# Optimization experiments

Hardware: AMD Instinct MI355X
Metric: run time of the kernel (lower is better)

## Reference

```python
import jax, jax.numpy as jnp
import numpy as np

N_NODES = 50000
N_EDGES = 800000
IN_FEATS = 64
K = 4
OUT_FEATS = 256


def setup_inputs() -> dict:
    key = jax.random.key(0)
    k1, k2, k3, k4, k5 = jax.random.split(key, 5)
    signal = jax.random.normal(k1, (N_NODES, IN_FEATS), dtype=jnp.float32)
    src = jax.random.randint(k2, (N_EDGES,), 0, N_NODES, dtype=jnp.int32)
    dst = jax.random.randint(k3, (N_EDGES,), 0, N_NODES, dtype=jnp.int32)
    lambda_max = jnp.array([2.0], dtype=jnp.float32)  # normalized Laplacian bound
    W = jax.random.normal(k4, (IN_FEATS * K, OUT_FEATS), dtype=jnp.float32) * (1.0 / np.sqrt(IN_FEATS * K))
    b = jax.random.normal(k5, (OUT_FEATS,), dtype=jnp.float32) * 0.01
    return {"signal": signal, "src": src, "dst": dst, "lambda_max": lambda_max, "W": W, "b": b}


def reference(signal, src, dst, lambda_max, W, b):
    n = signal.shape[0]
    # in-degrees, clamped to >= 1, then D^{-1/2}
    deg = jax.ops.segment_sum(jnp.ones_like(dst, dtype=signal.dtype), dst, num_segments=n)
    d_sqrt = jnp.power(jnp.clip(deg, 1.0), -0.5)[:, None]  # [N,1]

    def unn_laplacian(x):
        # D^{-1/2} A D^{-1/2} x via gather-from-src, scatter-sum-to-dst
        h = (x * d_sqrt)[src]                                   # [E,f]
        agg = jax.ops.segment_sum(h, dst, num_segments=n)       # [N,f]
        return agg * d_sqrt

    X0 = signal
    Xs = [X0]
    if K > 1:
        re_norm = 2.0 / lambda_max  # broadcasts over nodes ([1] -> [N,f])
        X1 = -re_norm * unn_laplacian(X0) + X0 * (re_norm - 1.0)
        Xs.append(X1)
        for _ in range(2, K):
            Xi = -2.0 * re_norm * unn_laplacian(X1) + X1 * 2.0 * (re_norm - 1.0) - X0
            Xs.append(Xi)
            X1, X0 = Xi, X1
    Xt = jnp.concatenate(Xs, axis=1)  # [N, f*K]
    return jax.nn.relu(Xt @ W + b)
```

## Files before the change

kernel.cpp:

```cpp
#include <hip/hip_runtime.h>

#define NN 50000
#define NE 800000
#define F  64
#define FK 256
#define OUTF 256
#define CAP 48
#define NT 3128

#define NPART 8
#define PART_NODES 6250
#define FILL_CHUNKS 256
#define CHUNK_E 3125

typedef __attribute__((ext_vector_type(8))) short s16x8;
typedef __attribute__((ext_vector_type(4))) float f32x4;

static __device__ __forceinline__ unsigned short f2bf(float f) {
    unsigned u = __float_as_uint(f);
    u += 0x7fffu + ((u >> 16) & 1u);
    return (unsigned short)(u >> 16);
}
static __device__ __forceinline__ float bf2f(int h) {
    return __uint_as_float(((unsigned)(h & 0xffff)) << 16);
}

__global__ __launch_bounds__(256) void fill_kernel(const int* __restrict__ src,
                                                   const int* __restrict__ dst,
                                                   int* __restrict__ cnt,
                                                   int* __restrict__ csr) {
    int part  = blockIdx.x & (NPART - 1);
    int chunk = blockIdx.x >> 3;
    int lo = part * PART_NODES;
    int e0 = chunk * CHUNK_E;
    int e1 = e0 + CHUNK_E;
    for (int e = e0 + threadIdx.x; e < e1; e += 256) {
        int d = dst[e];
        if ((unsigned)(d - lo) < (unsigned)PART_NODES) {
            int s = src[e];
            int k = atomicAdd(&cnt[d], 1);
            if (k < CAP) csr[d * CAP + k] = s;
        }
    }
}

__global__ void dsqrt_kernel(const int* __restrict__ cnt, float* __restrict__ dsq) {
    int n = blockIdx.x * blockDim.x + threadIdx.x;
    if (n < NN) dsq[n] = rsqrtf(fmaxf((float)cnt[n], 1.0f));
}


__global__ void copy0_kernel(const float* __restrict__ sig,
                             const float* __restrict__ dsq,
                             unsigned short* __restrict__ XrowH,
                             unsigned short* __restrict__ XrowL,
                             unsigned short* __restrict__ XfH) {
    int i = blockIdx.x * blockDim.x + threadIdx.x;
    if (i >= NN * 16) return;
    int n = i >> 4, fq = i & 15;
    float d = dsq[n];
    float4 v = *(const float4*)&sig[n * F + fq * 4];
    float yx = v.x * d, yy = v.y * d, yz = v.z * d, yw = v.w * d;
    unsigned short h0 = f2bf(yx), h1 = f2bf(yy), h2 = f2bf(yz), h3 = f2bf(yw);
    unsigned short l0 = f2bf(yx - bf2f(h0)), l1 = f2bf(yy - bf2f(h1));
    unsigned short l2 = f2bf(yz - bf2f(h2)), l3 = f2bf(yw - bf2f(h3));
    *(ushort4*)&XrowH[(size_t)n * 192 + fq * 4] = make_ushort4(h0, h1, h2, h3);
    *(ushort4*)&XrowL[(size_t)n * 192 + fq * 4] = make_ushort4(l0, l1, l2, l3);
    unsigned short u0 = f2bf(v.x), u1 = f2bf(v.y), u2 = f2bf(v.z), u3 = f2bf(v.w);
    int t = n >> 4, m = n & 15;
    int k0 = fq >> 3, qq = (fq >> 1) & 3, half = fq & 1;
    size_t base = ((size_t)((t * 8 + k0) * 64 + qq * 16 + m)) * 8 + half * 4;
    *(ushort4*)&XfH[base] = make_ushort4(u0, u1, u2, u3);
}

__global__ void convw_kernel(const float* __restrict__ W,
                             unsigned short* __restrict__ WfH,
                             unsigned short* __restrict__ WfL) {
    int id = blockIdx.x * blockDim.x + threadIdx.x;
    if (id >= 8192) return;
    int lane = id & 63, k0 = (id >> 6) & 7, ct = id >> 9;
    int n = lane & 15, q = lane >> 4;
    s16x8 h, l;
    #pragma unroll
    for (int j = 0; j < 8; ++j) {
        float x = W[(k0 * 32 + q * 8 + j) * OUTF + ct * 16 + n];
        unsigned short hh = f2bf(x);
        h[j] = (short)hh;
        l[j] = (short)f2bf(x - bf2f(hh));
    }
    ((s16x8*)WfH)[id] = h;
    ((s16x8*)WfL)[id] = l;
}

__global__ __launch_bounds__(256) void lap_kernel(const int* __restrict__ cnt,
                                                  const int* __restrict__ csr,
                                                  const float* __restrict__ dsq,
                                                  const float* __restrict__ lm,
                                                  unsigned short* __restrict__ XrowH,
                                                  unsigned short* __restrict__ XrowL,
                                                  unsigned short* __restrict__ XfH, int p) {
    int lane = threadIdx.x & 63;
    int half = lane >> 5;
    int sub  = lane & 31;
    int q2   = sub >> 4;
    int fq   = sub & 15;
    int wid  = (blockIdx.x * blockDim.x + threadIdx.x) >> 6;
    int n    = wid * 2 + half;
    if (n >= NN) return;
    int dgf = cnt[n];
    int dg  = min(dgf, CAP);
    int cin = p - 1;
    int foff = fq << 2;

    float ax = 0.f, ay = 0.f, az = 0.f, aw = 0.f;
    for (int k = 0; k < dg; k += 16) {
        int   s[8];
        float w[8];
        ushort4 h[8];
        #pragma unroll
        for (int j = 0; j < 8; ++j) {
            int slot = k + q2 + 2 * j;
            int ok   = slot < dg;
            int si   = csr[n * CAP + slot];
            s[j] = ok ? si : 0;
            w[j] = ok ? 1.0f : 0.0f;
        }
        #pragma unroll
        for (int j = 0; j < 8; ++j)
            h[j] = *(const ushort4*)&XrowH[((size_t)s[j] * 3 + cin) * 64 + foff];
        #pragma unroll
        for (int j = 0; j < 8; ++j) {
            ax += bf2f(h[j].x) * w[j];
            ay += bf2f(h[j].y) * w[j];
            az += bf2f(h[j].z) * w[j];
            aw += bf2f(h[j].w) * w[j];
        }
    }
    ax += __shfl_xor(ax, 16);
    ay += __shfl_xor(ay, 16);
    az += __shfl_xor(az, 16);
    aw += __shfl_xor(aw, 16);

    float rn = 2.0f / lm[0];
    float dn = dsq[n];
    float sq = sqrtf(fmaxf((float)dgf, 1.0f));
    ushort4 xh = *(const ushort4*)&XrowH[((size_t)n * 3 + cin) * 64 + foff];
    ushort4 xl = *(const ushort4*)&XrowL[((size_t)n * 3 + cin) * 64 + foff];
    float x1x = (bf2f(xh.x) + bf2f(xl.x)) * sq;
    float x1y = (bf2f(xh.y) + bf2f(xl.y)) * sq;
    float x1z = (bf2f(xh.z) + bf2f(xl.z)) * sq;
    float x1w = (bf2f(xh.w) + bf2f(xl.w)) * sq;
    float rx, ry, rz, rw;
    if (p == 1) {
        float c1 = rn - 1.0f;
        rx = -rn * dn * ax + x1x * c1;
        ry = -rn * dn * ay + x1y * c1;
        rz = -rn * dn * az + x1z * c1;
        rw = -rn * dn * aw + x1w * c1;
    } else {
        ushort4 zh = *(const ushort4*)&XrowH[((size_t)n * 3 + (p - 2)) * 64 + foff];
        ushort4 zl = *(const ushort4*)&XrowL[((size_t)n * 3 + (p - 2)) * 64 + foff];
        float c1 = 2.0f * (rn - 1.0f);
        rx = -2.0f * rn * dn * ax + x1x * c1 - (bf2f(zh.x) + bf2f(zl.x)) * sq;
        ry = -2.0f * rn * dn * ay + x1y * c1 - (bf2f(zh.y) + bf2f(zl.y)) * sq;
        rz = -2.0f * rn * dn * az + x1z * c1 - (bf2f(zh.z) + bf2f(zl.z)) * sq;
        rw = -2.0f * rn * dn * aw + x1w * c1 - (bf2f(zh.w) + bf2f(zl.w)) * sq;
    }

    float yx = rx * dn, yy = ry * dn, yz = rz * dn, yw = rw * dn;
    unsigned short yh0 = f2bf(yx), yh1 = f2bf(yy), yh2 = f2bf(yz), yh3 = f2bf(yw);
    if (q2 == 0) {
        if (p < 3)
            *(ushort4*)&XrowH[((size_t)n * 3 + p) * 64 + foff] = make_ushort4(yh0, yh1, yh2, yh3);
        unsigned short u0 = f2bf(rx), u1 = f2bf(ry), u2 = f2bf(rz), u3 = f2bf(rw);
        int t = n >> 4, m = n & 15;
        int k0 = p * 2 + (fq >> 3), qq = (fq >> 1) & 3, hf = fq & 1;
        size_t fbase = ((size_t)((t * 8 + k0) * 64 + qq * 16 + m)) * 8 + hf * 4;
        *(ushort4*)&XfH[fbase] = make_ushort4(u0, u1, u2, u3);
    } else if (p < 3) {
        unsigned short l0 = f2bf(yx - bf2f(yh0)), l1 = f2bf(yy - bf2f(yh1));
        unsigned short l2 = f2bf(yz - bf2f(yh2)), l3 = f2bf(yw - bf2f(yh3));
        *(ushort4*)&XrowL[((size_t)n * 3 + p) * 64 + foff] = make_ushort4(l0, l1, l2, l3);
    }
}

__global__ __launch_bounds__(512, 2) void gemm_kernel(const unsigned short* __restrict__ XfH,
                                                      const unsigned short* __restrict__ WfH,
                                                      const unsigned short* __restrict__ WfL,
                                                      const float* __restrict__ b,
                                                      float* __restrict__ out) {
    int lane = threadIdx.x & 63;
    int w    = threadIdx.x >> 6;
    int rh = w & 1, cg = w >> 1;
    int m = lane & 15, q = lane >> 4;
    int bt0 = blockIdx.x * 4;
    const s16x8* AH = (const s16x8*)XfH;
    const s16x8* BH = (const s16x8*)WfH;
    const s16x8* BL = (const s16x8*)WfL;

    f32x4 acc[2][4];
    #pragma unroll
    for (int rt = 0; rt < 2; ++rt)
        #pragma unroll
        for (int c = 0; c < 4; ++c) acc[rt][c] = (f32x4){0.f, 0.f, 0.f, 0.f};

    #pragma unroll
    for (int k0 = 0; k0 < 8; ++k0) {
        s16x8 a[2];
        #pragma unroll
        for (int rt = 0; rt < 2; ++rt)
            a[rt] = AH[((bt0 + rh * 2 + rt) * 8 + k0) * 64 + lane];
        #pragma unroll
        for (int c = 0; c < 4; ++c) {
            int ct = cg * 4 + c;
            s16x8 bh = BH[(ct * 8 + k0) * 64 + lane];
            s16x8 bl = BL[(ct * 8 + k0) * 64 + lane];
            #pragma unroll
            for (int rt = 0; rt < 2; ++rt) {
                acc[rt][c] = __builtin_amdgcn_mfma_f32_16x16x32_bf16(a[rt], bh, acc[rt][c], 0, 0, 0);
                acc[rt][c] = __builtin_amdgcn_mfma_f32_16x16x32_bf16(a[rt], bl, acc[rt][c], 0, 0, 0);
            }
        }
    }

    #pragma unroll
    for (int rt = 0; rt < 2; ++rt) {
        int rbase = (bt0 + rh * 2 + rt) * 16 + q * 4;
        #pragma unroll
        for (int c = 0; c < 4; ++c) {
            int col = (cg * 4 + c) * 16 + m;
            float bv = b[col];
            #pragma unroll
            for (int i = 0; i < 4; ++i) {
                int r = rbase + i;
                if (r < NN) out[r * OUTF + col] = fmaxf(acc[rt][c][i] + bv, 0.0f);
            }
        }
    }
}

extern "C" void kernel_launch(void* const* d_in, const int* in_sizes, int n_in,
                              void* d_out, int out_size, void* d_ws, size_t ws_size,
                              hipStream_t stream) {
    const float* signal     = (const float*)d_in[0];
    const int*   src        = (const int*)  d_in[1];
    const int*   dst        = (const int*)  d_in[2];
    const float* lambda_max = (const float*)d_in[3];
    const float* W          = (const float*)d_in[4];
    const float* b          = (const float*)d_in[5];
    float* out = (float*)d_out;

    int*   cnt = (int*)d_ws;
    int*   csr = cnt + NN;
    float* dsq = (float*)(csr + NN * CAP);
    unsigned short* XrowH = (unsigned short*)(dsq + NN);
    unsigned short* XrowL = XrowH + (size_t)NN * 192;
    unsigned short* XfH   = XrowL + (size_t)NN * 192;
    unsigned short* WfH   = XfH + (size_t)NT * 4096;
    unsigned short* WfL   = WfH + 65536;

    hipMemsetAsync(cnt, 0, NN * sizeof(int), stream);
    fill_kernel<<<NPART * FILL_CHUNKS, 256, 0, stream>>>(src, dst, cnt, csr);
    dsqrt_kernel<<<(NN + 255) / 256, 256, 0, stream>>>(cnt, dsq);
    copy0_kernel<<<(NN * 16 + 255) / 256, 256, 0, stream>>>(signal, dsq, XrowH, XrowL, XfH);
    convw_kernel<<<32, 256, 0, stream>>>(W, WfH, WfL);

    for (int p = 1; p <= 3; ++p)
        lap_kernel<<<NN / 8, 256, 0, stream>>>(cnt, csr, dsq, lambda_max, XrowH, XrowL, XfH, p);

    gemm_kernel<<<782, 512, 0, stream>>>(XfH, WfH, WfL, b, out);
}
```

Baseline: 232.7 us.

## Switch GEMM to single fp16 MFMA, fuse prep kernels, enlarge GEMM tile

The GEMM operands move from bf16 to fp16. W is no longer split into high and low bf16 halves, so the GEMM issues one MFMA per tile instead of two. The dsqrt, copy0 and convw kernels are merged into one prep kernel, and both prep and lap now recompute D^{-1/2} from the counts instead of reading a separate array. Each GEMM block now covers 8 row tiles instead of 4, so half as many blocks are launched. The fp16 path gives a narrower exponent range than bf16 and the larger tile increases register pressure and lowers the block count.

```diff
diff --git a/kernel.cpp b/kernel.cpp
--- a/kernel.cpp
+++ b/kernel.cpp
@@ -3,7 +3,6 @@
 #define NN 50000
 #define NE 800000
 #define F  64
-#define FK 256
 #define OUTF 256
 #define CAP 48
 #define NT 3128
@@ -13,8 +12,9 @@
 #define FILL_CHUNKS 256
 #define CHUNK_E 3125
 
-typedef __attribute__((ext_vector_type(8))) short s16x8;
-typedef __attribute__((ext_vector_type(4))) float f32x4;
+typedef __attribute__((ext_vector_type(8))) short    s16x8;
+typedef __attribute__((ext_vector_type(8))) _Float16 f16x8;
+typedef __attribute__((ext_vector_type(4))) float    f32x4;
 
 static __device__ __forceinline__ unsigned short f2bf(float f) {
     unsigned u = __float_as_uint(f);
@@ -23,6 +23,10 @@
 }
 static __device__ __forceinline__ float bf2f(int h) {
     return __uint_as_float(((unsigned)(h & 0xffff)) << 16);
+}
+static __device__ __forceinline__ unsigned short f2h(float f) {
+    _Float16 h = (_Float16)f;
+    return __builtin_bit_cast(unsigned short, h);
 }
 
 __global__ __launch_bounds__(256) void fill_kernel(const int* __restrict__ src,
@@ -44,61 +48,53 @@
     }
 }
 
-__global__ void dsqrt_kernel(const int* __restrict__ cnt, float* __restrict__ dsq) {
-    int n = blockIdx.x * blockDim.x + threadIdx.x;
-    if (n < NN) dsq[n] = rsqrtf(fmaxf((float)cnt[n], 1.0f));
-}
-
-
-__global__ void copy0_kernel(const float* __restrict__ sig,
-                             const float* __restrict__ dsq,
-                             unsigned short* __restrict__ XrowH,
-                             unsigned short* __restrict__ XrowL,
-                             unsigned short* __restrict__ XfH) {
-    int i = blockIdx.x * blockDim.x + threadIdx.x;
-    if (i >= NN * 16) return;
-    int n = i >> 4, fq = i & 15;
-    float d = dsq[n];
-    float4 v = *(const float4*)&sig[n * F + fq * 4];
-    float yx = v.x * d, yy = v.y * d, yz = v.z * d, yw = v.w * d;
-    unsigned short h0 = f2bf(yx), h1 = f2bf(yy), h2 = f2bf(yz), h3 = f2bf(yw);
-    unsigned short l0 = f2bf(yx - bf2f(h0)), l1 = f2bf(yy - bf2f(h1));
-    unsigned short l2 = f2bf(yz - bf2f(h2)), l3 = f2bf(yw - bf2f(h3));
-    *(ushort4*)&XrowH[(size_t)n * 192 + fq * 4] = make_ushort4(h0, h1, h2, h3);
-    *(ushort4*)&XrowL[(size_t)n * 192 + fq * 4] = make_ushort4(l0, l1, l2, l3);
-    unsigned short u0 = f2bf(v.x), u1 = f2bf(v.y), u2 = f2bf(v.z), u3 = f2bf(v.w);
-    int t = n >> 4, m = n & 15;
-    int k0 = fq >> 3, qq = (fq >> 1) & 3, half = fq & 1;
-    size_t base = ((size_t)((t * 8 + k0) * 64 + qq * 16 + m)) * 8 + half * 4;
-    *(ushort4*)&XfH[base] = make_ushort4(u0, u1, u2, u3);
-}
-
-__global__ void convw_kernel(const float* __restrict__ W,
-                             unsigned short* __restrict__ WfH,
-                             unsigned short* __restrict__ WfL) {
-    int id = blockIdx.x * blockDim.x + threadIdx.x;
-    if (id >= 8192) return;
-    int lane = id & 63, k0 = (id >> 6) & 7, ct = id >> 9;
-    int n = lane & 15, q = lane >> 4;
-    s16x8 h, l;
-    #pragma unroll
-    for (int j = 0; j < 8; ++j) {
-        float x = W[(k0 * 32 + q * 8 + j) * OUTF + ct * 16 + n];
-        unsigned short hh = f2bf(x);
-        h[j] = (short)hh;
-        l[j] = (short)f2bf(x - bf2f(hh));
-    }
-    ((s16x8*)WfH)[id] = h;
-    ((s16x8*)WfL)[id] = l;
+
+__global__ __launch_bounds__(256) void prep_kernel(const float* __restrict__ sig,
+                                                   const int* __restrict__ cnt,
+                                                   const float* __restrict__ W,
+                                                   unsigned short* __restrict__ XrowH,
+                                                   unsigned short* __restrict__ XrowL,
+                                                   unsigned short* __restrict__ XfF,
+                                                   unsigned short* __restrict__ WfF) {
+    int bid = blockIdx.x;
+    if (bid < 3125) {
+        int i = bid * 256 + threadIdx.x;
+        int n = i >> 4, fq = i & 15;
+        float d = rsqrtf(fmaxf((float)cnt[n], 1.0f));
+        float4 v = *(const float4*)&sig[n * F + fq * 4];
+        float yx = v.x * d, yy = v.y * d, yz = v.z * d, yw = v.w * d;
+        unsigned short h0 = f2bf(yx), h1 = f2bf(yy), h2 = f2bf(yz), h3 = f2bf(yw);
+        unsigned short l0 = f2bf(yx - bf2f(h0)), l1 = f2bf(yy - bf2f(h1));
+        unsigned short l2 = f2bf(yz - bf2f(h2)), l3 = f2bf(yw - bf2f(h3));
+        *(ushort4*)&XrowH[(size_t)n * 192 + fq * 4] = make_ushort4(h0, h1, h2, h3);
+        *(ushort4*)&XrowL[(size_t)n * 192 + fq * 4] = make_ushort4(l0, l1, l2, l3);
+        unsigned short u0 = f2h(v.x), u1 = f2h(v.y), u2 = f2h(v.z), u3 = f2h(v.w);
+        int t = n >> 4, m = n & 15;
+        int k0 = fq >> 3, qq = (fq >> 1) & 3, half = fq & 1;
+        size_t base = ((size_t)((t * 8 + k0) * 64 + qq * 16 + m)) * 8 + half * 4;
+        *(ushort4*)&XfF[base] = make_ushort4(u0, u1, u2, u3);
+    } else {
+        int id = (bid - 3125) * 256 + threadIdx.x;
+        if (id < 8192) {
+            int lane = id & 63, k0 = (id >> 6) & 7, ct = id >> 9;
+            int n = lane & 15, q = lane >> 4;
+            s16x8 h;
+            #pragma unroll
+            for (int j = 0; j < 8; ++j) {
+                float x = W[(k0 * 32 + q * 8 + j) * OUTF + ct * 16 + n];
+                h[j] = (short)f2h(x);
+            }
+            ((s16x8*)WfF)[id] = h;
+        }
+    }
 }
 
 __global__ __launch_bounds__(256) void lap_kernel(const int* __restrict__ cnt,
                                                   const int* __restrict__ csr,
-                                                  const float* __restrict__ dsq,
                                                   const float* __restrict__ lm,
                                                   unsigned short* __restrict__ XrowH,
                                                   unsigned short* __restrict__ XrowL,
-                                                  unsigned short* __restrict__ XfH, int p) {
+                                                  unsigned short* __restrict__ XfF, int p) {
     int lane = threadIdx.x & 63;
     int half = lane >> 5;
     int sub  = lane & 31;
@@ -142,7 +138,7 @@
     aw += __shfl_xor(aw, 16);
 
     float rn = 2.0f / lm[0];
-    float dn = dsq[n];
+    float dn = rsqrtf(fmaxf((float)dgf, 1.0f));
     float sq = sqrtf(fmaxf((float)dgf, 1.0f));
     ushort4 xh = *(const ushort4*)&XrowH[((size_t)n * 3 + cin) * 64 + foff];
     ushort4 xl = *(const ushort4*)&XrowL[((size_t)n * 3 + cin) * 64 + foff];
@@ -172,11 +168,11 @@
     if (q2 == 0) {
         if (p < 3)
             *(ushort4*)&XrowH[((size_t)n * 3 + p) * 64 + foff] = make_ushort4(yh0, yh1, yh2, yh3);
-        unsigned short u0 = f2bf(rx), u1 = f2bf(ry), u2 = f2bf(rz), u3 = f2bf(rw);
+        unsigned short u0 = f2h(rx), u1 = f2h(ry), u2 = f2h(rz), u3 = f2h(rw);
         int t = n >> 4, m = n & 15;
         int k0 = p * 2 + (fq >> 3), qq = (fq >> 1) & 3, hf = fq & 1;
         size_t fbase = ((size_t)((t * 8 + k0) * 64 + qq * 16 + m)) * 8 + hf * 4;
-        *(ushort4*)&XfH[fbase] = make_ushort4(u0, u1, u2, u3);
+        *(ushort4*)&XfF[fbase] = make_ushort4(u0, u1, u2, u3);
     } else if (p < 3) {
         unsigned short l0 = f2bf(yx - bf2f(yh0)), l1 = f2bf(yy - bf2f(yh1));
         unsigned short l2 = f2bf(yz - bf2f(yh2)), l3 = f2bf(yw - bf2f(yh3));
@@ -184,48 +180,43 @@
     }
 }
 
-__global__ __launch_bounds__(512, 2) void gemm_kernel(const unsigned short* __restrict__ XfH,
-                                                      const unsigned short* __restrict__ WfH,
-                                                      const unsigned short* __restrict__ WfL,
+__global__ __launch_bounds__(512, 2) void gemm_kernel(const unsigned short* __restrict__ XfF,
+                                                      const unsigned short* __restrict__ WfF,
                                                       const float* __restrict__ b,
                                                       float* __restrict__ out) {
     int lane = threadIdx.x & 63;
     int w    = threadIdx.x >> 6;
     int rh = w & 1, cg = w >> 1;
     int m = lane & 15, q = lane >> 4;
-    int bt0 = blockIdx.x * 4;
-    const s16x8* AH = (const s16x8*)XfH;
-    const s16x8* BH = (const s16x8*)WfH;
-    const s16x8* BL = (const s16x8*)WfL;
-
-    f32x4 acc[2][4];
+    int bt0 = blockIdx.x * 8;
+    const f16x8* A = (const f16x8*)XfF;
+    const f16x8* B = (const f16x8*)WfF;
+
+    f32x4 acc[4][4];
     #pragma unroll
-    for (int rt = 0; rt < 2; ++rt)
+    for (int rt = 0; rt < 4; ++rt)
         #pragma unroll
         for (int c = 0; c < 4; ++c) acc[rt][c] = (f32x4){0.f, 0.f, 0.f, 0.f};
 
     #pragma unroll
     for (int k0 = 0; k0 < 8; ++k0) {
-        s16x8 a[2];
-        #pragma unroll
-        for (int rt = 0; rt < 2; ++rt)
-            a[rt] = AH[((bt0 + rh * 2 + rt) * 8 + k0) * 64 + lane];
+        f16x8 a[4];
+        #pragma unroll
+        for (int rt = 0; rt < 4; ++rt)
+            a[rt] = A[((bt0 + rh * 4 + rt) * 8 + k0) * 64 + lane];
         #pragma unroll
         for (int c = 0; c < 4; ++c) {
             int ct = cg * 4 + c;
-            s16x8 bh = BH[(ct * 8 + k0) * 64 + lane];
-            s16x8 bl = BL[(ct * 8 + k0) * 64 + lane];
+            f16x8 bh = B[(ct * 8 + k0) * 64 + lane];
             #pragma unroll
-            for (int rt = 0; rt < 2; ++rt) {
-                acc[rt][c] = __builtin_amdgcn_mfma_f32_16x16x32_bf16(a[rt], bh, acc[rt][c], 0, 0, 0);
-                acc[rt][c] = __builtin_amdgcn_mfma_f32_16x16x32_bf16(a[rt], bl, acc[rt][c], 0, 0, 0);
-            }
+            for (int rt = 0; rt < 4; ++rt)
+                acc[rt][c] = __builtin_amdgcn_mfma_f32_16x16x32_f16(a[rt], bh, acc[rt][c], 0, 0, 0);
         }
     }
 
     #pragma unroll
-    for (int rt = 0; rt < 2; ++rt) {
-        int rbase = (bt0 + rh * 2 + rt) * 16 + q * 4;
+    for (int rt = 0; rt < 4; ++rt) {
+        int rbase = (bt0 + rh * 4 + rt) * 16 + q * 4;
         #pragma unroll
         for (int c = 0; c < 4; ++c) {
             int col = (cg * 4 + c) * 16 + m;
@@ -252,21 +243,17 @@
 
     int*   cnt = (int*)d_ws;
     int*   csr = cnt + NN;
-    float* dsq = (float*)(csr + NN * CAP);
-    unsigned short* XrowH = (unsigned short*)(dsq + NN);
+    unsigned short* XrowH = (unsigned short*)(csr + NN * CAP);
     unsigned short* XrowL = XrowH + (size_t)NN * 192;
-    unsigned short* XfH   = XrowL + (size_t)NN * 192;
-    unsigned short* WfH   = XfH + (size_t)NT * 4096;
-    unsigned short* WfL   = WfH + 65536;
+    unsigned short* XfF   = XrowL + (size_t)NN * 192;
+    unsigned short* WfF   = XfF + (size_t)NT * 4096;
 
     hipMemsetAsync(cnt, 0, NN * sizeof(int), stream);
     fill_kernel<<<NPART * FILL_CHUNKS, 256, 0, stream>>>(src, dst, cnt, csr);
-    dsqrt_kernel<<<(NN + 255) / 256, 256, 0, stream>>>(cnt, dsq);
-    copy0_kernel<<<(NN * 16 + 255) / 256, 256, 0, stream>>>(signal, dsq, XrowH, XrowL, XfH);
-    convw_kernel<<<32, 256, 0, stream>>>(W, WfH, WfL);
+    prep_kernel<<<3125 + 32, 256, 0, stream>>>(signal, cnt, W, XrowH, XrowL, XfF, WfF);
 
     for (int p = 1; p <= 3; ++p)
-        lap_kernel<<<NN / 8, 256, 0, stream>>>(cnt, csr, dsq, lambda_max, XrowH, XrowL, XfH, p);
-
-    gemm_kernel<<<782, 512, 0, stream>>>(XfH, WfH, WfL, b, out);
-}
+        lap_kernel<<<NN / 8, 256, 0, stream>>>(cnt, csr, lambda_max, XrowH, XrowL, XfF, p);
+
+    gemm_kernel<<<391, 512, 0, stream>>>(XfF, WfF, b, out);
+}
```

New measurement: 252.7 us. 1.09x slower.
